# Kernel optimization log

Measured on AMD Instinct MI355X. Metric: run time of the kernel, lower is better.

The kernel has to match this reference:

```python
import jax, jax.numpy as jnp
import numpy as np

N_NODES = 100000
N_EDGES = 1600000
EMBED_DIM = 128
HIDDEN_DIM = 256


def setup_inputs() -> dict:
    key = jax.random.key(0)
    k_emb, k_src, k_dst, k_w1, k_w2 = jax.random.split(key, 5)
    emb = jax.random.normal(k_emb, (N_NODES, EMBED_DIM), dtype=jnp.float32)
    edge_src = jax.random.randint(k_src, (N_EDGES,), 0, N_NODES)
    edge_dst = jax.random.randint(k_dst, (N_EDGES,), 0, N_NODES)
    # Linear(2D -> H) and Linear(H -> D), stored as [in, out] for x @ W
    W1 = jax.random.normal(k_w1, (2 * EMBED_DIM, HIDDEN_DIM), dtype=jnp.float32) * (1.0 / np.sqrt(2 * EMBED_DIM))
    b1 = jnp.zeros((HIDDEN_DIM,), dtype=jnp.float32)
    W2 = jax.random.normal(k_w2, (HIDDEN_DIM, EMBED_DIM), dtype=jnp.float32) * (1.0 / np.sqrt(HIDDEN_DIM))
    b2 = jnp.zeros((EMBED_DIM,), dtype=jnp.float32)
    return {"emb": emb, "edge_src": edge_src, "edge_dst": edge_dst,
            "W1": W1, "b1": b1, "W2": W2, "b2": b2}


def reference(emb, edge_src, edge_dst, W1, b1, W2, b2):
    N, D = emb.shape
    E = edge_src.shape[0]
    # gather neighbor embeddings and segment-mean per destination node
    gathered = emb[edge_src]                                    # [E, D]
    nbr_sum = jax.ops.segment_sum(gathered, edge_dst, num_segments=N)   # [N, D]
    counts = jax.ops.segment_sum(jnp.ones((E,), emb.dtype), edge_dst, num_segments=N)  # [N]
    nbr_mean = nbr_sum / jnp.maximum(counts, 1.0)[:, None]
    # nodes with no neighbors fall back to their own embedding
    nbr_mean = jnp.where(counts[:, None] == 0, emb, nbr_mean)
    concat = jnp.concatenate([emb, nbr_mean], axis=-1)          # [N, 2D]
    h = jax.nn.relu(concat @ W1 + b1)                           # [N, H]
    return h @ W2 + b2                                          # [N, D]
```

## Files before the change

kernel.cpp:

```cpp
#include <hip/hip_runtime.h>

#define DD 128
#define HH 256
#define K1 256
#define BM 64
#define CH 2048
#define CH1 4096
#define CAP 8192

typedef __bf16 bf16;
typedef __attribute__((ext_vector_type(8))) __bf16 bf16x8;
typedef __attribute__((ext_vector_type(4))) float f32x4;
typedef __attribute__((ext_vector_type(2))) float f32x2;


__global__ __launch_bounds__(256) void count512_k(const int* __restrict__ dst,
                                                  int* __restrict__ bcnt,
                                                  int E, int BSH) {
    __shared__ int c[512];
    for (int j = threadIdx.x; j < 512; j += 256) c[j] = 0;
    __syncthreads();
    for (int e = blockIdx.x * 256 + threadIdx.x; e < E; e += gridDim.x * 256)
        atomicAdd(&c[dst[e] >> BSH], 1);
    __syncthreads();
    for (int j = threadIdx.x; j < 512; j += 256)
        if (c[j]) atomicAdd(&bcnt[j], c[j]);
}

__global__ __launch_bounds__(512) void scan512_k(const int* __restrict__ bcnt,
                                                 int* __restrict__ bbase,
                                                 int* __restrict__ bpos,
                                                 int NB, int E) {
    __shared__ int s[512];
    const int t = threadIdx.x;
    int v = (t < NB) ? bcnt[t] : 0;
    s[t] = v;
    __syncthreads();
    for (int off = 1; off < 512; off <<= 1) {
        int y = (t >= off) ? s[t - off] : 0;
        __syncthreads();
        s[t] += y;
        __syncthreads();
    }
    int excl = s[t] - v;
    if (t < NB) { bbase[t] = excl; bpos[t] = excl; }
    if (t == 0) bbase[NB] = E;
}

__global__ __launch_bounds__(256) void part512_k(const int* __restrict__ src,
                                                 const int* __restrict__ dst,
                                                 int* __restrict__ bpos,
                                                 int2* __restrict__ pairs,
                                                 int E, int BSH) {
    __shared__ int lcnt[512];
    __shared__ int lbase[512];
    const int t = threadIdx.x;
    const int e0 = blockIdx.x * CH1;
    const int e1 = min(E, e0 + CH1);
    for (int j = t; j < 512; j += 256) lcnt[j] = 0;
    __syncthreads();
    int rs[CH1 / 256];
    #pragma unroll
    for (int k = 0; k < CH1 / 256; ++k) {
        int e = e0 + k * 256 + t;
        int b = -1;
        if (e < e1) { b = dst[e] >> BSH; atomicAdd(&lcnt[b], 1); }
        rs[k] = b;
    }
    __syncthreads();
    for (int j = t; j < 512; j += 256) {
        int c = lcnt[j];
        lbase[j] = c ? atomicAdd(&bpos[j], c) : 0;
        lcnt[j] = 0;
    }
    __syncthreads();
    #pragma unroll
    for (int k = 0; k < CH1 / 256; ++k) {
        int e = e0 + k * 256 + t;
        if (e < e1) {
            int b = rs[k];
            int slot = lbase[b] + atomicAdd(&lcnt[b], 1);
            pairs[slot] = make_int2(src[e], dst[e]);
        }
    }
}

__global__ __launch_bounds__(256) void sortb_k(const int2* __restrict__ pairs,
                                               const int* __restrict__ bbase,
                                               int* __restrict__ offs,
                                               int* __restrict__ ssrc,
                                               int N, int BSH) {
    __shared__ int hist[512];
    __shared__ int pref[512];
    __shared__ int run[512];
    __shared__ int sorted[CAP];
    const int t = threadIdx.x;
    const int b = blockIdx.x;
    const int B = 1 << BSH;
    const int d0 = b << BSH;
    const int nd = min(B, N - d0);
    const int rb = bbase[b], re = bbase[b + 1];
    const int cntE = re - rb;
    for (int j = t; j < 512; j += 256) hist[j] = 0;
    __syncthreads();
    for (int i = rb + t; i < re; i += 256)
        atomicAdd(&hist[pairs[i].y - d0], 1);
    __syncthreads();
    for (int j = t; j < 512; j += 256) pref[j] = hist[j];
    __syncthreads();
    for (int off = 1; off < 512; off <<= 1) {
        int j2 = t + 256;
        int v0 = (t >= off) ? pref[t - off] : 0;
        int v1 = (j2 >= off) ? pref[j2 - off] : 0;
        __syncthreads();
        pref[t] += v0;
        pref[j2] += v1;
        __syncthreads();
    }
    for (int j = t; j < nd; j += 256) offs[d0 + j] = rb + pref[j];
    for (int j = t; j < 512; j += 256) run[j] = pref[j] - hist[j];
    __syncthreads();
    if (cntE <= CAP) {
        for (int i = rb + t; i < re; i += 256) {
            int2 p = pairs[i];
            int pos = atomicAdd(&run[p.y - d0], 1);
            sorted[pos] = p.x;
        }
        __syncthreads();
        for (int i = t; i < cntE; i += 256) ssrc[rb + i] = sorted[i];
    } else {
        for (int i = rb + t; i < re; i += 256) {
            int2 p = pairs[i];
            int pos = atomicAdd(&run[p.y - d0], 1);
            ssrc[rb + pos] = p.x;
        }
    }
}


__global__ __launch_bounds__(256) void hist_k(const int* __restrict__ dst,
                                              int* __restrict__ cnt, int E) {
    for (int e = blockIdx.x * blockDim.x + threadIdx.x; e < E;
         e += gridDim.x * blockDim.x)
        atomicAdd(&cnt[dst[e]], 1);
}

__global__ __launch_bounds__(256) void scan1_k(const int* __restrict__ cnt,
                                               int* __restrict__ offs,
                                               int* __restrict__ part, int N) {
    __shared__ int sdata[256];
    const int b = blockIdx.x, t = threadIdx.x;
    const int base = b * 1024 + t * 4;
    int v[4], sum = 0;
    #pragma unroll
    for (int i = 0; i < 4; ++i) {
        int idx = base + i;
        v[i] = (idx < N) ? cnt[idx] : 0;
        sum += v[i];
    }
    sdata[t] = sum;
    __syncthreads();
    for (int off = 1; off < 256; off <<= 1) {
        int y = (t >= off) ? sdata[t - off] : 0;
        __syncthreads();
        sdata[t] += y;
        __syncthreads();
    }
    int excl = sdata[t] - sum;
    if (t == 255) part[b] = sdata[255];
    int run = excl;
    #pragma unroll
    for (int i = 0; i < 4; ++i) {
        int idx = base + i;
        if (idx < N) offs[idx] = run;
        run += v[i];
    }
}

__global__ __launch_bounds__(128) void scan2_k(int* __restrict__ part, int nparts) {
    __shared__ int sdata[128];
    const int t = threadIdx.x;
    int v = (t < nparts) ? part[t] : 0;
    sdata[t] = v;
    __syncthreads();
    for (int off = 1; off < 128; off <<= 1) {
        int y = (t >= off) ? sdata[t - off] : 0;
        __syncthreads();
        sdata[t] += y;
        __syncthreads();
    }
    if (t < nparts) part[t] = sdata[t] - v;
}

__global__ __launch_bounds__(256) void scan3_k(int* __restrict__ offs,
                                               const int* __restrict__ part, int N) {
    for (int i = blockIdx.x * blockDim.x + threadIdx.x; i < N;
         i += gridDim.x * blockDim.x)
        offs[i] += part[i >> 10];
}

__global__ __launch_bounds__(256) void bucket_k(const int* __restrict__ src,
                                                const int* __restrict__ dst,
                                                int* __restrict__ offs,
                                                int* __restrict__ ssrc,
                                                int E, int N) {
    const int r = blockIdx.x & 7;
    const int chunk = blockIdx.x >> 3;
    const int lo = r * (N >> 3);
    const int hi = (r == 7) ? N : lo + (N >> 3);
    const int e0 = chunk * CH;
    const int e1 = min(E, e0 + CH);
    for (int e = e0 + threadIdx.x; e < e1; e += 256) {
        int d = dst[e];
        if (d >= lo && d < hi) {
            int pos = atomicAdd(&offs[d], 1);
            ssrc[pos] = src[e];
        }
    }
}

__global__ __launch_bounds__(256) void cvt8_k(const float* __restrict__ emb,
                                              unsigned* __restrict__ emb8,
                                              size_t n8) {
    for (size_t i = blockIdx.x * blockDim.x + threadIdx.x; i < n8;
         i += (size_t)gridDim.x * blockDim.x) {
        float4 a = *reinterpret_cast<const float4*>(&emb[i * 8]);
        float4 b = *reinterpret_cast<const float4*>(&emb[i * 8 + 4]);
        int w0 = __builtin_amdgcn_cvt_pk_fp8_f32(a.x, a.y, 0, false);
        w0 = __builtin_amdgcn_cvt_pk_fp8_f32(a.z, a.w, w0, true);
        int w1 = __builtin_amdgcn_cvt_pk_fp8_f32(b.x, b.y, 0, false);
        w1 = __builtin_amdgcn_cvt_pk_fp8_f32(b.z, b.w, w1, true);
        uint2 o; o.x = (unsigned)w0; o.y = (unsigned)w1;
        *reinterpret_cast<uint2*>(&emb8[i * 2]) = o;
    }
}

__global__ __launch_bounds__(256) void gather8_k(const unsigned* __restrict__ emb8,
                                                 const float* __restrict__ emb,
                                                 const int* __restrict__ offs,
                                                 const int* __restrict__ ssrc,
                                                 bf16* __restrict__ nbrh, int N) {
    const int wid = threadIdx.x >> 6;
    const int lane = threadIdx.x & 63;
    const int d = blockIdx.x * 4 + wid;
    if (d >= N) return;
    const int slot = lane >> 4;
    const int c8 = (lane & 15) * 8;
    const int start = (d == 0) ? 0 : offs[d - 1];
    const int end = offs[d];
    float acc[8];
    #pragma unroll
    for (int j = 0; j < 8; ++j) acc[j] = 0.f;
    int e = start;
    for (; e + 8 <= end; e += 8) {
        int s0 = ssrc[e + slot];
        int s1 = ssrc[e + 4 + slot];
        uint2 v0 = *reinterpret_cast<const uint2*>(&emb8[((size_t)s0 * DD + c8) >> 2]);
        uint2 v1 = *reinterpret_cast<const uint2*>(&emb8[((size_t)s1 * DD + c8) >> 2]);
        f32x2 p;
        p = __builtin_amdgcn_cvt_pk_f32_fp8(v0.x, false); acc[0] += p[0]; acc[1] += p[1];
        p = __builtin_amdgcn_cvt_pk_f32_fp8(v0.x, true);  acc[2] += p[0]; acc[3] += p[1];
        p = __builtin_amdgcn_cvt_pk_f32_fp8(v0.y, false); acc[4] += p[0]; acc[5] += p[1];
        p = __builtin_amdgcn_cvt_pk_f32_fp8(v0.y, true);  acc[6] += p[0]; acc[7] += p[1];
        p = __builtin_amdgcn_cvt_pk_f32_fp8(v1.x, false); acc[0] += p[0]; acc[1] += p[1];
        p = __builtin_amdgcn_cvt_pk_f32_fp8(v1.x, true);  acc[2] += p[0]; acc[3] += p[1];
        p = __builtin_amdgcn_cvt_pk_f32_fp8(v1.y, false); acc[4] += p[0]; acc[5] += p[1];
        p = __builtin_amdgcn_cvt_pk_f32_fp8(v1.y, true);  acc[6] += p[0]; acc[7] += p[1];
    }
    for (; e + 4 <= end; e += 4) {
        int s0 = ssrc[e + slot];
        uint2 v0 = *reinterpret_cast<const uint2*>(&emb8[((size_t)s0 * DD + c8) >> 2]);
        f32x2 p;
        p = __builtin_amdgcn_cvt_pk_f32_fp8(v0.x, false); acc[0] += p[0]; acc[1] += p[1];
        p = __builtin_amdgcn_cvt_pk_f32_fp8(v0.x, true);  acc[2] += p[0]; acc[3] += p[1];
        p = __builtin_amdgcn_cvt_pk_f32_fp8(v0.y, false); acc[4] += p[0]; acc[5] += p[1];
        p = __builtin_amdgcn_cvt_pk_f32_fp8(v0.y, true);  acc[6] += p[0]; acc[7] += p[1];
    }
    if (slot < end - e) {
        int s0 = ssrc[e + slot];
        uint2 v0 = *reinterpret_cast<const uint2*>(&emb8[((size_t)s0 * DD + c8) >> 2]);
        f32x2 p;
        p = __builtin_amdgcn_cvt_pk_f32_fp8(v0.x, false); acc[0] += p[0]; acc[1] += p[1];
        p = __builtin_amdgcn_cvt_pk_f32_fp8(v0.x, true);  acc[2] += p[0]; acc[3] += p[1];
        p = __builtin_amdgcn_cvt_pk_f32_fp8(v0.y, false); acc[4] += p[0]; acc[5] += p[1];
        p = __builtin_amdgcn_cvt_pk_f32_fp8(v0.y, true);  acc[6] += p[0]; acc[7] += p[1];
    }
    #pragma unroll
    for (int j = 0; j < 8; ++j) {
        acc[j] += __shfl_xor(acc[j], 16);
        acc[j] += __shfl_xor(acc[j], 32);
    }
    if (slot == 0) {
        bf16x8 o;
        if (end > start) {
            float inv = 1.f / (float)(end - start);
            #pragma unroll
            for (int j = 0; j < 8; ++j) o[j] = (bf16)(acc[j] * inv);
        } else {
            float4 a = *reinterpret_cast<const float4*>(&emb[(size_t)d * DD + c8]);
            float4 b = *reinterpret_cast<const float4*>(&emb[(size_t)d * DD + c8 + 4]);
            o[0]=(bf16)a.x; o[1]=(bf16)a.y; o[2]=(bf16)a.z; o[3]=(bf16)a.w;
            o[4]=(bf16)b.x; o[5]=(bf16)b.y; o[6]=(bf16)b.z; o[7]=(bf16)b.w;
        }
        *reinterpret_cast<bf16x8*>(&nbrh[(size_t)d * DD + c8]) = o;
    }
}

__global__ __launch_bounds__(256) void gather_k(const float* __restrict__ emb,
                                                const int* __restrict__ offs,
                                                const int* __restrict__ ssrc,
                                                float* __restrict__ nbr, int N) {
    const int wid = threadIdx.x >> 6;
    const int lane = threadIdx.x & 63;
    const int d = blockIdx.x * 4 + wid;
    if (d >= N) return;
    const int sub = lane >> 5;
    const int c = (lane & 31) * 4;
    const int start = (d == 0) ? 0 : offs[d - 1];
    const int end = offs[d];
    float4 acc = make_float4(0.f, 0.f, 0.f, 0.f);
    int e = start;
    for (; e + 4 <= end; e += 4) {
        int s0 = ssrc[e + sub];
        int s1 = ssrc[e + 2 + sub];
        float4 v0 = *reinterpret_cast<const float4*>(&emb[(size_t)s0 * DD + c]);
        float4 v1 = *reinterpret_cast<const float4*>(&emb[(size_t)s1 * DD + c]);
        acc.x += v0.x + v1.x; acc.y += v0.y + v1.y;
        acc.z += v0.z + v1.z; acc.w += v0.w + v1.w;
    }
    for (; e + 2 <= end; e += 2) {
        int s = ssrc[e + sub];
        float4 v = *reinterpret_cast<const float4*>(&emb[(size_t)s * DD + c]);
        acc.x += v.x; acc.y += v.y; acc.z += v.z; acc.w += v.w;
    }
    if (e < end && sub == 0) {
        int s = ssrc[e];
        float4 v = *reinterpret_cast<const float4*>(&emb[(size_t)s * DD + c]);
        acc.x += v.x; acc.y += v.y; acc.z += v.z; acc.w += v.w;
    }
    acc.x += __shfl_xor(acc.x, 32);
    acc.y += __shfl_xor(acc.y, 32);
    acc.z += __shfl_xor(acc.z, 32);
    acc.w += __shfl_xor(acc.w, 32);
    if (sub == 0) {
        if (end > start) {
            float inv = 1.f / (float)(end - start);
            acc.x *= inv; acc.y *= inv; acc.z *= inv; acc.w *= inv;
        } else {
            acc = *reinterpret_cast<const float4*>(&emb[(size_t)d * DD + c]);
        }
        *reinterpret_cast<float4*>(&nbr[(size_t)d * DD + c]) = acc;
    }
}

__global__ __launch_bounds__(64) void pack_k(const float* __restrict__ W, int NC,
                                             bf16* __restrict__ hi) {
    const int ntiles = NC >> 4;
    const int kt = blockIdx.x / ntiles;
    const int nt = blockIdx.x % ntiles;
    const int l = threadIdx.x;
    const int k0 = kt * 32 + (l >> 4) * 8;
    const int n = nt * 16 + (l & 15);
    bf16x8 hv;
    #pragma unroll
    for (int r = 0; r < 8; ++r)
        hv[r] = (bf16)W[(size_t)(k0 + r) * NC + n];
    *reinterpret_cast<bf16x8*>(hi + ((size_t)blockIdx.x * 64 + l) * 8) = hv;
}

__global__ __launch_bounds__(256) void mlp_mfma_k(const float* __restrict__ emb,
        const float* nbrf, const bf16* __restrict__ nbrh,
        const bf16* __restrict__ w1h, const float* __restrict__ b1,
        const bf16* __restrict__ w2h, const float* __restrict__ b2,
        float* out, int N) {
    __shared__ char smem[BM * K1 * 2];
    const int t = threadIdx.x;
    const int n0 = blockIdx.x * BM;
    const int l = t & 63;
    const int w = t >> 6;

    #pragma unroll
    for (int i = 0; i < 8; ++i) {
        int chunk = i * 256 + t;
        int row = chunk >> 5;
        int c0 = (chunk & 31) * 8;
        int n = n0 + row;
        bf16x8 hv;
        if (n < N) {
            if (c0 >= DD && nbrh != nullptr) {
                hv = *reinterpret_cast<const bf16x8*>(&nbrh[(size_t)n * DD + (c0 - DD)]);
            } else {
                const float* sp = (c0 < DD) ? &emb[(size_t)n * DD + c0]
                                            : &nbrf[(size_t)n * DD + (c0 - DD)];
                float4 a = *reinterpret_cast<const float4*>(sp);
                float4 b = *reinterpret_cast<const float4*>(sp + 4);
                hv[0]=(bf16)a.x; hv[1]=(bf16)a.y; hv[2]=(bf16)a.z; hv[3]=(bf16)a.w;
                hv[4]=(bf16)b.x; hv[5]=(bf16)b.y; hv[6]=(bf16)b.z; hv[7]=(bf16)b.w;
            }
        } else {
            #pragma unroll
            for (int j = 0; j < 8; ++j) hv[j] = (bf16)0.f;
        }
        int off = row * 512 + ((c0 * 2) ^ ((row & 7) << 4));
        *reinterpret_cast<bf16x8*>(smem + off) = hv;
    }
    __syncthreads();

    const int arow = l & 15;
    const int abyte = (l >> 4) * 16;

    f32x4 acc[4][4];
    #pragma unroll
    for (int ntl = 0; ntl < 4; ++ntl) {
        float bv = b1[w * 64 + ntl * 16 + (l & 15)];
        #pragma unroll
        for (int mt = 0; mt < 4; ++mt)
            acc[mt][ntl] = (f32x4){bv, bv, bv, bv};
    }
    for (int kt = 0; kt < 8; ++kt) {
        bf16x8 ah[4];
        #pragma unroll
        for (int mt = 0; mt < 4; ++mt) {
            int row = mt * 16 + arow;
            int off = row * 512 + ((kt * 64 + abyte) ^ ((row & 7) << 4));
            ah[mt] = *reinterpret_cast<const bf16x8*>(smem + off);
        }
        #pragma unroll
        for (int ntl = 0; ntl < 4; ++ntl) {
            int nt = w * 4 + ntl;
            size_t boff = ((size_t)(kt * 16 + nt) * 64 + l) * 8;
            bf16x8 bh = *reinterpret_cast<const bf16x8*>(w1h + boff);
            #pragma unroll
            for (int mt = 0; mt < 4; ++mt)
                acc[mt][ntl] = __builtin_amdgcn_mfma_f32_16x16x32_bf16(ah[mt], bh, acc[mt][ntl], 0, 0, 0);
        }
    }
    __syncthreads();

    #pragma unroll
    for (int mt = 0; mt < 4; ++mt)
        #pragma unroll
        for (int ntl = 0; ntl < 4; ++ntl) {
            int col = w * 64 + ntl * 16 + (l & 15);
            #pragma unroll
            for (int r = 0; r < 4; ++r) {
                int row = mt * 16 + (l >> 4) * 4 + r;
                int off = row * 512 + ((col * 2) ^ ((row & 7) << 4));
                *reinterpret_cast<bf16*>(smem + off) = (bf16)fmaxf(acc[mt][ntl][r], 0.f);
            }
        }
    __syncthreads();

    f32x4 acc2[4][2];
    #pragma unroll
    for (int ntl = 0; ntl < 2; ++ntl) {
        float bv = b2[w * 32 + ntl * 16 + (l & 15)];
        #pragma unroll
        for (int mt = 0; mt < 4; ++mt)
            acc2[mt][ntl] = (f32x4){bv, bv, bv, bv};
    }
    for (int kt = 0; kt < 8; ++kt) {
        bf16x8 ah[4];
        #pragma unroll
        for (int mt = 0; mt < 4; ++mt) {
            int row = mt * 16 + arow;
            int off = row * 512 + ((kt * 64 + abyte) ^ ((row & 7) << 4));
            ah[mt] = *reinterpret_cast<const bf16x8*>(smem + off);
        }
        #pragma unroll
        for (int ntl = 0; ntl < 2; ++ntl) {
            int nt = w * 2 + ntl;
            size_t boff = ((size_t)(kt * 8 + nt) * 64 + l) * 8;
            bf16x8 bh = *reinterpret_cast<const bf16x8*>(w2h + boff);
            #pragma unroll
            for (int mt = 0; mt < 4; ++mt)
                acc2[mt][ntl] = __builtin_amdgcn_mfma_f32_16x16x32_bf16(ah[mt], bh, acc2[mt][ntl], 0, 0, 0);
        }
    }
    #pragma unroll
    for (int mt = 0; mt < 4; ++mt)
        #pragma unroll
        for (int ntl = 0; ntl < 2; ++ntl) {
            int col = w * 32 + ntl * 16 + (l & 15);
            #pragma unroll
            for (int r = 0; r < 4; ++r) {
                int row = mt * 16 + (l >> 4) * 4 + r;
                int n = n0 + row;
                if (n < N) out[(size_t)n * DD + col] = acc2[mt][ntl][r];
            }
        }
}

__global__ __launch_bounds__(256) void scatter_k(const float* __restrict__ emb,
        const int* __restrict__ src, const int* __restrict__ dst,
        float* nbr, float* __restrict__ cnt, int E) {
    int e = blockIdx.x * 8 + (threadIdx.x >> 5);
    if (e >= E) return;
    int lane = threadIdx.x & 31;
    int s = src[e];
    int d = dst[e];
    const float4 v = *reinterpret_cast<const float4*>(&emb[(size_t)s * DD + lane * 4]);
    float* o = &nbr[(size_t)d * DD + lane * 4];
    atomicAdd(o + 0, v.x);
    atomicAdd(o + 1, v.y);
    atomicAdd(o + 2, v.z);
    atomicAdd(o + 3, v.w);
    if (lane == 0) atomicAdd(&cnt[d], 1.0f);
}

__global__ __launch_bounds__(256) void mlp_k(const float* __restrict__ emb,
        const float* nbr, const float* cnt,
        const float* __restrict__ W1, const float* __restrict__ b1,
        const float* __restrict__ W2, const float* __restrict__ b2,
        float* out, int N) {
    __shared__ float smem[BM * K1];
    const int t = threadIdx.x;
    const int n0 = blockIdx.x * BM;
    #pragma unroll
    for (int it = 0; it < 16; ++it) {
        int idx = it * 256 + t;
        int r = idx >> 6;
        int c4 = idx & 63;
        int n = n0 + r;
        float4 v = make_float4(0.f, 0.f, 0.f, 0.f);
        if (n < N) {
            if (c4 < 32) {
                v = *reinterpret_cast<const float4*>(&emb[(size_t)n * DD + c4 * 4]);
            } else {
                float c = cnt[n];
                if (c > 0.f) {
                    v = *reinterpret_cast<const float4*>(&nbr[(size_t)n * DD + (c4 - 32) * 4]);
                    float inv = 1.f / c;
                    v.x *= inv; v.y *= inv; v.z *= inv; v.w *= inv;
                } else {
                    v = *reinterpret_cast<const float4*>(&emb[(size_t)n * DD + (c4 - 32) * 4]);
                }
            }
        }
        *reinterpret_cast<float4*>(&smem[idx * 4]) = v;
    }
    __syncthreads();
    const int tx = t & 31;
    const int ty = t >> 5;
    const int r0 = ty * 8;
    {
        const int c0 = tx * 8;
        float acc[8][8];
        const float4 bva = *reinterpret_cast<const float4*>(&b1[c0]);
        const float4 bvb = *reinterpret_cast<const float4*>(&b1[c0 + 4]);
        #pragma unroll
        for (int i = 0; i < 8; ++i) {
            acc[i][0] = bva.x; acc[i][1] = bva.y; acc[i][2] = bva.z; acc[i][3] = bva.w;
            acc[i][4] = bvb.x; acc[i][5] = bvb.y; acc[i][6] = bvb.z; acc[i][7] = bvb.w;
        }
        for (int k0 = 0; k0 < K1; k0 += 4) {
            float xs[8][4];
            #pragma unroll
            for (int i = 0; i < 8; ++i) {
                float4 xv = *reinterpret_cast<const float4*>(&smem[(r0 + i) * K1 + k0]);
                xs[i][0] = xv.x; xs[i][1] = xv.y; xs[i][2] = xv.z; xs[i][3] = xv.w;
            }
            #pragma unroll
            for (int kk = 0; kk < 4; ++kk) {
                const float4 wa = *reinterpret_cast<const float4*>(&W1[(size_t)(k0 + kk) * HH + c0]);
                const float4 wb = *reinterpret_cast<const float4*>(&W1[(size_t)(k0 + kk) * HH + c0 + 4]);
                #pragma unroll
                for (int i = 0; i < 8; ++i) {
                    float x = xs[i][kk];
                    acc[i][0] += x * wa.x; acc[i][1] += x * wa.y;
                    acc[i][2] += x * wa.z; acc[i][3] += x * wa.w;
                    acc[i][4] += x * wb.x; acc[i][5] += x * wb.y;
                    acc[i][6] += x * wb.z; acc[i][7] += x * wb.w;
                }
            }
        }
        __syncthreads();
        #pragma unroll
        for (int i = 0; i < 8; ++i) {
            float4 h0, h1;
            h0.x = fmaxf(acc[i][0], 0.f); h0.y = fmaxf(acc[i][1], 0.f);
            h0.z = fmaxf(acc[i][2], 0.f); h0.w = fmaxf(acc[i][3], 0.f);
            h1.x = fmaxf(acc[i][4], 0.f); h1.y = fmaxf(acc[i][5], 0.f);
            h1.z = fmaxf(acc[i][6], 0.f); h1.w = fmaxf(acc[i][7], 0.f);
            *reinterpret_cast<float4*>(&smem[(r0 + i) * HH + c0]) = h0;
            *reinterpret_cast<float4*>(&smem[(r0 + i) * HH + c0 + 4]) = h1;
        }
        __syncthreads();
    }
    {
        const int c0 = tx * 4;
        float acc[8][4];
        const float4 bv = *reinterpret_cast<const float4*>(&b2[c0]);
        #pragma unroll
        for (int i = 0; i < 8; ++i) {
            acc[i][0] = bv.x; acc[i][1] = bv.y; acc[i][2] = bv.z; acc[i][3] = bv.w;
        }
        for (int k0 = 0; k0 < HH; k0 += 4) {
            float hs[8][4];
            #pragma unroll
            for (int i = 0; i < 8; ++i) {
                float4 hv = *reinterpret_cast<const float4*>(&smem[(r0 + i) * HH + k0]);
                hs[i][0] = hv.x; hs[i][1] = hv.y; hs[i][2] = hv.z; hs[i][3] = hv.w;
            }
            #pragma unroll
            for (int kk = 0; kk < 4; ++kk) {
                const float4 w2 = *reinterpret_cast<const float4*>(&W2[(size_t)(k0 + kk) * DD + c0]);
                #pragma unroll
                for (int i = 0; i < 8; ++i) {
                    float h = hs[i][kk];
                    acc[i][0] += h * w2.x; acc[i][1] += h * w2.y;
                    acc[i][2] += h * w2.z; acc[i][3] += h * w2.w;
                }
            }
        }
        #pragma unroll
        for (int i = 0; i < 8; ++i) {
            int n = n0 + r0 + i;
            if (n < N) {
                float4 o;
                o.x = acc[i][0]; o.y = acc[i][1]; o.z = acc[i][2]; o.w = acc[i][3];
                *reinterpret_cast<float4*>(&out[(size_t)n * DD + c0]) = o;
            }
        }
    }
}

extern "C" void kernel_launch(void* const* d_in, const int* in_sizes, int n_in,
                              void* d_out, int out_size, void* d_ws, size_t ws_size,
                              hipStream_t stream) {
    const float* emb = (const float*)d_in[0];
    const int* esrc  = (const int*)d_in[1];
    const int* edst  = (const int*)d_in[2];
    const float* W1  = (const float*)d_in[3];
    const float* b1  = (const float*)d_in[4];
    const float* W2  = (const float*)d_in[5];
    const float* b2  = (const float*)d_in[6];
    float* out = (float*)d_out;

    const int N = in_sizes[0] / DD;
    const int E = in_sizes[1];
    const int nparts = (N + 1023) / 1024;

    int BSH = 0;
    while ((((size_t)N + ((size_t)1 << BSH) - 1) >> BSH) > 512) ++BSH;
    const int B = 1 << BSH;
    const int NB = (N + B - 1) >> BSH;

    int* cnt  = (int*)d_ws;
    int* offs = cnt + N;
    int* part = offs + N;
    int* aux  = part + 128;
    int* ssrc = aux + 2048;
    char* wp = (char*)(ssrc + E);
    wp = (char*)(((uintptr_t)wp + 15) & ~(uintptr_t)15);
    bf16* w1h = (bf16*)wp;
    bf16* w2h = w1h + 65536;
    unsigned* emb8 = (unsigned*)(w2h + 32768);
    bf16* nbrh = (bf16*)(emb8 + (size_t)N * DD / 4);
    int2* pairs = (int2*)nbrh;
    int* bcnt  = aux;
    int* bbase = aux + 512;
    int* bpos  = aux + 1280;
    const size_t need_base = (size_t)((char*)(w2h + 32768) - (char*)d_ws);
    const size_t need_full = (size_t)((char*)(nbrh + (size_t)N * DD) - (char*)d_ws);
    const bool pairs_fit = ((size_t)E * sizeof(int2) <= (size_t)N * DD * sizeof(bf16));

    if (ws_size >= need_base && nparts <= 128) {
        const bool fast = (ws_size >= need_full) && pairs_fit && (B <= 512) && ((N & 7) == 0);
        pack_k<<<dim3(128), dim3(64), 0, stream>>>(W1, HH, w1h);
        pack_k<<<dim3(64), dim3(64), 0, stream>>>(W2, DD, w2h);
        if (fast) {
            hipMemsetAsync(bcnt, 0, 512 * sizeof(int), stream);
            count512_k<<<dim3(512), dim3(256), 0, stream>>>(edst, bcnt, E, BSH);
            scan512_k<<<dim3(1), dim3(512), 0, stream>>>(bcnt, bbase, bpos, NB, E);
            part512_k<<<dim3((E + CH1 - 1) / CH1), dim3(256), 0, stream>>>(
                esrc, edst, bpos, pairs, E, BSH);
            sortb_k<<<dim3(NB), dim3(256), 0, stream>>>(pairs, bbase, offs, ssrc, N, BSH);
            cvt8_k<<<dim3(2048), dim3(256), 0, stream>>>(emb, emb8, (size_t)N * DD / 8);
            gather8_k<<<dim3((N + 3) / 4), dim3(256), 0, stream>>>(emb8, emb, offs, ssrc, nbrh, N);
            mlp_mfma_k<<<dim3((N + BM - 1) / BM), dim3(256), 0, stream>>>(
                emb, nullptr, nbrh, w1h, b1, w2h, b2, out, N);
        } else {
            hipMemsetAsync(cnt, 0, (size_t)N * sizeof(int), stream);
            hist_k<<<dim3(1024), dim3(256), 0, stream>>>(edst, cnt, E);
            scan1_k<<<dim3(nparts), dim3(256), 0, stream>>>(cnt, offs, part, N);
            scan2_k<<<dim3(1), dim3(128), 0, stream>>>(part, nparts);
            scan3_k<<<dim3(512), dim3(256), 0, stream>>>(offs, part, N);
            const int nchunks = (E + CH - 1) / CH;
            bucket_k<<<dim3(nchunks * 8), dim3(256), 0, stream>>>(esrc, edst, offs, ssrc, E, N);
            gather_k<<<dim3((N + 3) / 4), dim3(256), 0, stream>>>(emb, offs, ssrc, out, N);
            mlp_mfma_k<<<dim3((N + BM - 1) / BM), dim3(256), 0, stream>>>(
                emb, out, nullptr, w1h, b1, w2h, b2, out, N);
        }
    } else {
        float* fcnt = (float*)d_ws;
        hipMemsetAsync(out, 0, (size_t)N * DD * sizeof(float), stream);
        hipMemsetAsync(fcnt, 0, (size_t)N * sizeof(float), stream);
        scatter_k<<<dim3((E + 7) / 8), dim3(256), 0, stream>>>(emb, esrc, edst, out, fcnt, E);
        mlp_k<<<dim3((N + BM - 1) / BM), dim3(256), 0, stream>>>(
            emb, out, fcnt, W1, b1, W2, b2, out, N);
    }
}
```

Before: 173.0 us.

## Fuse neighbor gather into MLP kernel and pack edge pairs into 32 bits

The fp8 neighbor gather/mean now runs inside the MLP kernel and writes straight into the shared-memory A tile, so the bf16 neighbor buffer round trip and one launch are gone. Edge pairs are packed into one 32-bit word (local dst in the top 8 bits, src in the low 24), which halves partition and sort traffic and lets pairs reuse the emb8 buffer. The two weight-pack launches are merged into one. In exchange, the gather now runs at one block per 64 nodes with serial iterations before the MFMA work, which may hide memory latency less well. The fast path is also limited to N < 2^24 and buckets of at most 256 nodes.

```diff
diff --git a/kernel.cpp b/kernel.cpp
--- a/kernel.cpp
+++ b/kernel.cpp
@@ -50,8 +50,8 @@
 __global__ __launch_bounds__(256) void part512_k(const int* __restrict__ src,
                                                  const int* __restrict__ dst,
                                                  int* __restrict__ bpos,
-                                                 int2* __restrict__ pairs,
-                                                 int E, int BSH) {
+                                                 unsigned* __restrict__ pairs,
+                                                 int E, int BSH, int Bm1) {
     __shared__ int lcnt[512];
     __shared__ int lbase[512];
     const int t = threadIdx.x;
@@ -80,12 +80,12 @@
         if (e < e1) {
             int b = rs[k];
             int slot = lbase[b] + atomicAdd(&lcnt[b], 1);
-            pairs[slot] = make_int2(src[e], dst[e]);
-        }
-    }
-}
-
-__global__ __launch_bounds__(256) void sortb_k(const int2* __restrict__ pairs,
+            pairs[slot] = ((unsigned)(dst[e] & Bm1) << 24) | (unsigned)src[e];
+        }
+    }
+}
+
+__global__ __launch_bounds__(256) void sortb_k(const unsigned* __restrict__ pairs,
                                                const int* __restrict__ bbase,
                                                int* __restrict__ offs,
                                                int* __restrict__ ssrc,
@@ -104,7 +104,7 @@
     for (int j = t; j < 512; j += 256) hist[j] = 0;
     __syncthreads();
     for (int i = rb + t; i < re; i += 256)
-        atomicAdd(&hist[pairs[i].y - d0], 1);
+        atomicAdd(&hist[pairs[i] >> 24], 1);
     __syncthreads();
     for (int j = t; j < 512; j += 256) pref[j] = hist[j];
     __syncthreads();
@@ -122,17 +122,17 @@
     __syncthreads();
     if (cntE <= CAP) {
         for (int i = rb + t; i < re; i += 256) {
-            int2 p = pairs[i];
-            int pos = atomicAdd(&run[p.y - d0], 1);
-            sorted[pos] = p.x;
+            unsigned p = pairs[i];
+            int pos = atomicAdd(&run[p >> 24], 1);
+            sorted[pos] = (int)(p & 0xFFFFFFu);
         }
         __syncthreads();
         for (int i = t; i < cntE; i += 256) ssrc[rb + i] = sorted[i];
     } else {
         for (int i = rb + t; i < re; i += 256) {
-            int2 p = pairs[i];
-            int pos = atomicAdd(&run[p.y - d0], 1);
-            ssrc[rb + pos] = p.x;
+            unsigned p = pairs[i];
+            int pos = atomicAdd(&run[p >> 24], 1);
+            ssrc[rb + pos] = (int)(p & 0xFFFFFFu);
         }
     }
 }
@@ -216,93 +216,6 @@
             int pos = atomicAdd(&offs[d], 1);
             ssrc[pos] = src[e];
         }
-    }
-}
-
-__global__ __launch_bounds__(256) void cvt8_k(const float* __restrict__ emb,
-                                              unsigned* __restrict__ emb8,
-                                              size_t n8) {
-    for (size_t i = blockIdx.x * blockDim.x + threadIdx.x; i < n8;
-         i += (size_t)gridDim.x * blockDim.x) {
-        float4 a = *reinterpret_cast<const float4*>(&emb[i * 8]);
-        float4 b = *reinterpret_cast<const float4*>(&emb[i * 8 + 4]);
-        int w0 = __builtin_amdgcn_cvt_pk_fp8_f32(a.x, a.y, 0, false);
-        w0 = __builtin_amdgcn_cvt_pk_fp8_f32(a.z, a.w, w0, true);
-        int w1 = __builtin_amdgcn_cvt_pk_fp8_f32(b.x, b.y, 0, false);
-        w1 = __builtin_amdgcn_cvt_pk_fp8_f32(b.z, b.w, w1, true);
-        uint2 o; o.x = (unsigned)w0; o.y = (unsigned)w1;
-        *reinterpret_cast<uint2*>(&emb8[i * 2]) = o;
-    }
-}
-
-__global__ __launch_bounds__(256) void gather8_k(const unsigned* __restrict__ emb8,
-                                                 const float* __restrict__ emb,
-                                                 const int* __restrict__ offs,
-                                                 const int* __restrict__ ssrc,
-                                                 bf16* __restrict__ nbrh, int N) {
-    const int wid = threadIdx.x >> 6;
-    const int lane = threadIdx.x & 63;
-    const int d = blockIdx.x * 4 + wid;
-    if (d >= N) return;
-    const int slot = lane >> 4;
-    const int c8 = (lane & 15) * 8;
-    const int start = (d == 0) ? 0 : offs[d - 1];
-    const int end = offs[d];
-    float acc[8];
-    #pragma unroll
-    for (int j = 0; j < 8; ++j) acc[j] = 0.f;
-    int e = start;
-    for (; e + 8 <= end; e += 8) {
-        int s0 = ssrc[e + slot];
-        int s1 = ssrc[e + 4 + slot];
-        uint2 v0 = *reinterpret_cast<const uint2*>(&emb8[((size_t)s0 * DD + c8) >> 2]);
-        uint2 v1 = *reinterpret_cast<const uint2*>(&emb8[((size_t)s1 * DD + c8) >> 2]);
-        f32x2 p;
-        p = __builtin_amdgcn_cvt_pk_f32_fp8(v0.x, false); acc[0] += p[0]; acc[1] += p[1];
-        p = __builtin_amdgcn_cvt_pk_f32_fp8(v0.x, true);  acc[2] += p[0]; acc[3] += p[1];
-        p = __builtin_amdgcn_cvt_pk_f32_fp8(v0.y, false); acc[4] += p[0]; acc[5] += p[1];
-        p = __builtin_amdgcn_cvt_pk_f32_fp8(v0.y, true);  acc[6] += p[0]; acc[7] += p[1];
-        p = __builtin_amdgcn_cvt_pk_f32_fp8(v1.x, false); acc[0] += p[0]; acc[1] += p[1];
-        p = __builtin_amdgcn_cvt_pk_f32_fp8(v1.x, true);  acc[2] += p[0]; acc[3] += p[1];
-        p = __builtin_amdgcn_cvt_pk_f32_fp8(v1.y, false); acc[4] += p[0]; acc[5] += p[1];
-        p = __builtin_amdgcn_cvt_pk_f32_fp8(v1.y, true);  acc[6] += p[0]; acc[7] += p[1];
-    }
-    for (; e + 4 <= end; e += 4) {
-        int s0 = ssrc[e + slot];
-        uint2 v0 = *reinterpret_cast<const uint2*>(&emb8[((size_t)s0 * DD + c8) >> 2]);
-        f32x2 p;
-        p = __builtin_amdgcn_cvt_pk_f32_fp8(v0.x, false); acc[0] += p[0]; acc[1] += p[1];
-        p = __builtin_amdgcn_cvt_pk_f32_fp8(v0.x, true);  acc[2] += p[0]; acc[3] += p[1];
-        p = __builtin_amdgcn_cvt_pk_f32_fp8(v0.y, false); acc[4] += p[0]; acc[5] += p[1];
-        p = __builtin_amdgcn_cvt_pk_f32_fp8(v0.y, true);  acc[6] += p[0]; acc[7] += p[1];
-    }
-    if (slot < end - e) {
-        int s0 = ssrc[e + slot];
-        uint2 v0 = *reinterpret_cast<const uint2*>(&emb8[((size_t)s0 * DD + c8) >> 2]);
-        f32x2 p;
-        p = __builtin_amdgcn_cvt_pk_f32_fp8(v0.x, false); acc[0] += p[0]; acc[1] += p[1];
-        p = __builtin_amdgcn_cvt_pk_f32_fp8(v0.x, true);  acc[2] += p[0]; acc[3] += p[1];
-        p = __builtin_amdgcn_cvt_pk_f32_fp8(v0.y, false); acc[4] += p[0]; acc[5] += p[1];
-        p = __builtin_amdgcn_cvt_pk_f32_fp8(v0.y, true);  acc[6] += p[0]; acc[7] += p[1];
-    }
-    #pragma unroll
-    for (int j = 0; j < 8; ++j) {
-        acc[j] += __shfl_xor(acc[j], 16);
-        acc[j] += __shfl_xor(acc[j], 32);
-    }
-    if (slot == 0) {
-        bf16x8 o;
-        if (end > start) {
-            float inv = 1.f / (float)(end - start);
-            #pragma unroll
-            for (int j = 0; j < 8; ++j) o[j] = (bf16)(acc[j] * inv);
-        } else {
-            float4 a = *reinterpret_cast<const float4*>(&emb[(size_t)d * DD + c8]);
-            float4 b = *reinterpret_cast<const float4*>(&emb[(size_t)d * DD + c8 + 4]);
-            o[0]=(bf16)a.x; o[1]=(bf16)a.y; o[2]=(bf16)a.z; o[3]=(bf16)a.w;
-            o[4]=(bf16)b.x; o[5]=(bf16)b.y; o[6]=(bf16)b.z; o[7]=(bf16)b.w;
-        }
-        *reinterpret_cast<bf16x8*>(&nbrh[(size_t)d * DD + c8]) = o;
     }
 }
 
@@ -353,11 +266,33 @@
     }
 }
 
-__global__ __launch_bounds__(64) void pack_k(const float* __restrict__ W, int NC,
-                                             bf16* __restrict__ hi) {
+__global__ __launch_bounds__(256) void cvt8_k(const float* __restrict__ emb,
+                                              unsigned* __restrict__ emb8,
+                                              size_t n8) {
+    for (size_t i = blockIdx.x * blockDim.x + threadIdx.x; i < n8;
+         i += (size_t)gridDim.x * blockDim.x) {
+        float4 a = *reinterpret_cast<const float4*>(&emb[i * 8]);
+        float4 b = *reinterpret_cast<const float4*>(&emb[i * 8 + 4]);
+        int w0 = __builtin_amdgcn_cvt_pk_fp8_f32(a.x, a.y, 0, false);
+        w0 = __builtin_amdgcn_cvt_pk_fp8_f32(a.z, a.w, w0, true);
+        int w1 = __builtin_amdgcn_cvt_pk_fp8_f32(b.x, b.y, 0, false);
+        w1 = __builtin_amdgcn_cvt_pk_fp8_f32(b.z, b.w, w1, true);
+        uint2 o; o.x = (unsigned)w0; o.y = (unsigned)w1;
+        *reinterpret_cast<uint2*>(&emb8[i * 2]) = o;
+    }
+}
+
+__global__ __launch_bounds__(64) void packW_k(const float* __restrict__ W1,
+                                              const float* __restrict__ W2,
+                                              bf16* __restrict__ w1h,
+                                              bf16* __restrict__ w2h) {
+    const int bid = blockIdx.x;
+    const float* W; bf16* outp; int NC; int rel;
+    if (bid < 128) { W = W1; outp = w1h; NC = HH; rel = bid; }
+    else           { W = W2; outp = w2h; NC = DD; rel = bid - 128; }
     const int ntiles = NC >> 4;
-    const int kt = blockIdx.x / ntiles;
-    const int nt = blockIdx.x % ntiles;
+    const int kt = rel / ntiles;
+    const int nt = rel % ntiles;
     const int l = threadIdx.x;
     const int k0 = kt * 32 + (l >> 4) * 8;
     const int n = nt * 16 + (l & 15);
@@ -365,11 +300,201 @@
     #pragma unroll
     for (int r = 0; r < 8; ++r)
         hv[r] = (bf16)W[(size_t)(k0 + r) * NC + n];
-    *reinterpret_cast<bf16x8*>(hi + ((size_t)blockIdx.x * 64 + l) * 8) = hv;
+    *reinterpret_cast<bf16x8*>(outp + ((size_t)rel * 64 + l) * 8) = hv;
+}
+
+__global__ __launch_bounds__(256) void mlp_fused_k(const float* __restrict__ emb,
+        const unsigned* __restrict__ emb8,
+        const int* __restrict__ offs, const int* __restrict__ ssrc,
+        const bf16* __restrict__ w1h, const float* __restrict__ b1,
+        const bf16* __restrict__ w2h, const float* __restrict__ b2,
+        float* __restrict__ out, int N) {
+    __shared__ char smem[BM * K1 * 2];
+    const int t = threadIdx.x;
+    const int n0 = blockIdx.x * BM;
+    const int l = t & 63;
+    const int w = t >> 6;
+
+    #pragma unroll
+    for (int i = 0; i < 4; ++i) {
+        int chunk = i * 256 + t;
+        int row = chunk >> 4;
+        int c0 = (chunk & 15) * 8;
+        int n = n0 + row;
+        bf16x8 hv;
+        if (n < N) {
+            float4 a = *reinterpret_cast<const float4*>(&emb[(size_t)n * DD + c0]);
+            float4 b = *reinterpret_cast<const float4*>(&emb[(size_t)n * DD + c0 + 4]);
+            hv[0]=(bf16)a.x; hv[1]=(bf16)a.y; hv[2]=(bf16)a.z; hv[3]=(bf16)a.w;
+            hv[4]=(bf16)b.x; hv[5]=(bf16)b.y; hv[6]=(bf16)b.z; hv[7]=(bf16)b.w;
+        } else {
+            #pragma unroll
+            for (int j = 0; j < 8; ++j) hv[j] = (bf16)0.f;
+        }
+        int off = row * 512 + ((c0 * 2) ^ ((row & 7) << 4));
+        *reinterpret_cast<bf16x8*>(smem + off) = hv;
+    }
+
+    {
+        const int slot = l >> 4;
+        const int c8 = (l & 15) * 8;
+        for (int it = 0; it < 16; ++it) {
+            int row = it * 4 + w;
+            int d = n0 + row;
+            bf16x8 o;
+            #pragma unroll
+            for (int j = 0; j < 8; ++j) o[j] = (bf16)0.f;
+            if (d < N) {
+                const int start = (d == 0) ? 0 : offs[d - 1];
+                const int end = offs[d];
+                float acc[8];
+                #pragma unroll
+                for (int j = 0; j < 8; ++j) acc[j] = 0.f;
+                int e = start;
+                for (; e + 8 <= end; e += 8) {
+                    int s0 = ssrc[e + slot];
+                    int s1 = ssrc[e + 4 + slot];
+                    uint2 v0 = *reinterpret_cast<const uint2*>(&emb8[((size_t)s0 * DD + c8) >> 2]);
+                    uint2 v1 = *reinterpret_cast<const uint2*>(&emb8[((size_t)s1 * DD + c8) >> 2]);
+                    f32x2 p;
+                    p = __builtin_amdgcn_cvt_pk_f32_fp8(v0.x, false); acc[0] += p[0]; acc[1] += p[1];
+                    p = __builtin_amdgcn_cvt_pk_f32_fp8(v0.x, true);  acc[2] += p[0]; acc[3] += p[1];
+                    p = __builtin_amdgcn_cvt_pk_f32_fp8(v0.y, false); acc[4] += p[0]; acc[5] += p[1];
+                    p = __builtin_amdgcn_cvt_pk_f32_fp8(v0.y, true);  acc[6] += p[0]; acc[7] += p[1];
+                    p = __builtin_amdgcn_cvt_pk_f32_fp8(v1.x, false); acc[0] += p[0]; acc[1] += p[1];
+                    p = __builtin_amdgcn_cvt_pk_f32_fp8(v1.x, true);  acc[2] += p[0]; acc[3] += p[1];
+                    p = __builtin_amdgcn_cvt_pk_f32_fp8(v1.y, false); acc[4] += p[0]; acc[5] += p[1];
+                    p = __builtin_amdgcn_cvt_pk_f32_fp8(v1.y, true);  acc[6] += p[0]; acc[7] += p[1];
+                }
+                for (; e + 4 <= end; e += 4) {
+                    int s0 = ssrc[e + slot];
+                    uint2 v0 = *reinterpret_cast<const uint2*>(&emb8[((size_t)s0 * DD + c8) >> 2]);
+                    f32x2 p;
+                    p = __builtin_amdgcn_cvt_pk_f32_fp8(v0.x, false); acc[0] += p[0]; acc[1] += p[1];
+                    p = __builtin_amdgcn_cvt_pk_f32_fp8(v0.x, true);  acc[2] += p[0]; acc[3] += p[1];
+                    p = __builtin_amdgcn_cvt_pk_f32_fp8(v0.y, false); acc[4] += p[0]; acc[5] += p[1];
+                    p = __builtin_amdgcn_cvt_pk_f32_fp8(v0.y, true);  acc[6] += p[0]; acc[7] += p[1];
+                }
+                if (slot < end - e) {
+                    int s0 = ssrc[e + slot];
+                    uint2 v0 = *reinterpret_cast<const uint2*>(&emb8[((size_t)s0 * DD + c8) >> 2]);
+                    f32x2 p;
+                    p = __builtin_amdgcn_cvt_pk_f32_fp8(v0.x, false); acc[0] += p[0]; acc[1] += p[1];
+                    p = __builtin_amdgcn_cvt_pk_f32_fp8(v0.x, true);  acc[2] += p[0]; acc[3] += p[1];
+                    p = __builtin_amdgcn_cvt_pk_f32_fp8(v0.y, false); acc[4] += p[0]; acc[5] += p[1];
+                    p = __builtin_amdgcn_cvt_pk_f32_fp8(v0.y, true);  acc[6] += p[0]; acc[7] += p[1];
+                }
+                #pragma unroll
+                for (int j = 0; j < 8; ++j) {
+                    acc[j] += __shfl_xor(acc[j], 16);
+                    acc[j] += __shfl_xor(acc[j], 32);
+                }
+                if (end > start) {
+                    float inv = 1.f / (float)(end - start);
+                    #pragma unroll
+                    for (int j = 0; j < 8; ++j) o[j] = (bf16)(acc[j] * inv);
+                } else {
+                    float4 a = *reinterpret_cast<const float4*>(&emb[(size_t)d * DD + c8]);
+                    float4 b = *reinterpret_cast<const float4*>(&emb[(size_t)d * DD + c8 + 4]);
+                    o[0]=(bf16)a.x; o[1]=(bf16)a.y; o[2]=(bf16)a.z; o[3]=(bf16)a.w;
+                    o[4]=(bf16)b.x; o[5]=(bf16)b.y; o[6]=(bf16)b.z; o[7]=(bf16)b.w;
+                }
+            }
+            if (slot == 0) {
+                int off = row * 512 + (((DD + c8) * 2) ^ ((row & 7) << 4));
+                *reinterpret_cast<bf16x8*>(smem + off) = o;
+            }
+        }
+    }
+    __syncthreads();
+
+    const int arow = l & 15;
+    const int abyte = (l >> 4) * 16;
+
+    f32x4 acc[4][4];
+    #pragma unroll
+    for (int ntl = 0; ntl < 4; ++ntl) {
+        float bv = b1[w * 64 + ntl * 16 + (l & 15)];
+        #pragma unroll
+        for (int mt = 0; mt < 4; ++mt)
+            acc[mt][ntl] = (f32x4){bv, bv, bv, bv};
+    }
+    for (int kt = 0; kt < 8; ++kt) {
+        bf16x8 ah[4];
+        #pragma unroll
+        for (int mt = 0; mt < 4; ++mt) {
+            int row = mt * 16 + arow;
+            int off = row * 512 + ((kt * 64 + abyte) ^ ((row & 7) << 4));
+            ah[mt] = *reinterpret_cast<const bf16x8*>(smem + off);
+        }
+        #pragma unroll
+        for (int ntl = 0; ntl < 4; ++ntl) {
+            int nt = w * 4 + ntl;
+            size_t boff = ((size_t)(kt * 16 + nt) * 64 + l) * 8;
+            bf16x8 bh = *reinterpret_cast<const bf16x8*>(w1h + boff);
+            #pragma unroll
+            for (int mt = 0; mt < 4; ++mt)
+                acc[mt][ntl] = __builtin_amdgcn_mfma_f32_16x16x32_bf16(ah[mt], bh, acc[mt][ntl], 0, 0, 0);
+        }
+    }
+    __syncthreads();
+
+    #pragma unroll
+    for (int mt = 0; mt < 4; ++mt)
+        #pragma unroll
+        for (int ntl = 0; ntl < 4; ++ntl) {
+            int col = w * 64 + ntl * 16 + (l & 15);
+            #pragma unroll
+            for (int r = 0; r < 4; ++r) {
+                int row = mt * 16 + (l >> 4) * 4 + r;
+                int off = row * 512 + ((col * 2) ^ ((row & 7) << 4));
+                *reinterpret_cast<bf16*>(smem + off) = (bf16)fmaxf(acc[mt][ntl][r], 0.f);
+            }
+        }
+    __syncthreads();
+
+    f32x4 acc2[4][2];
+    #pragma unroll
+    for (int ntl = 0; ntl < 2; ++ntl) {
+        float bv = b2[w * 32 + ntl * 16 + (l & 15)];
+        #pragma unroll
+        for (int mt = 0; mt < 4; ++mt)
+            acc2[mt][ntl] = (f32x4){bv, bv, bv, bv};
+    }
+    for (int kt = 0; kt < 8; ++kt) {
+        bf16x8 ah[4];
+        #pragma unroll
+        for (int mt = 0; mt < 4; ++mt) {
+            int row = mt * 16 + arow;
+            int off = row * 512 + ((kt * 64 + abyte) ^ ((row & 7) << 4));
+            ah[mt] = *reinterpret_cast<const bf16x8*>(smem + off);
+        }
+        #pragma unroll
+        for (int ntl = 0; ntl < 2; ++ntl) {
+            int nt = w * 2 + ntl;
+            size_t boff = ((size_t)(kt * 8 + nt) * 64 + l) * 8;
+            bf16x8 bh = *reinterpret_cast<const bf16x8*>(w2h + boff);
+            #pragma unroll
+            for (int mt = 0; mt < 4; ++mt)
+                acc2[mt][ntl] = __builtin_amdgcn_mfma_f32_16x16x32_bf16(ah[mt], bh, acc2[mt][ntl], 0, 0, 0);
+        }
+    }
+    #pragma unroll
+    for (int mt = 0; mt < 4; ++mt)
+        #pragma unroll
+        for (int ntl = 0; ntl < 2; ++ntl) {
+            int col = w * 32 + ntl * 16 + (l & 15);
+            #pragma unroll
+            for (int r = 0; r < 4; ++r) {
+                int row = mt * 16 + (l >> 4) * 4 + r;
+                int n = n0 + row;
+                if (n < N) out[(size_t)n * DD + col] = acc2[mt][ntl][r];
+            }
+        }
 }
 
 __global__ __launch_bounds__(256) void mlp_mfma_k(const float* __restrict__ emb,
-        const float* nbrf, const bf16* __restrict__ nbrh,
+        const float* nbrf,
         const bf16* __restrict__ w1h, const float* __restrict__ b1,
         const bf16* __restrict__ w2h, const float* __restrict__ b2,
         float* out, int N) {
@@ -387,16 +512,12 @@
         int n = n0 + row;
         bf16x8 hv;
         if (n < N) {
-            if (c0 >= DD && nbrh != nullptr) {
-                hv = *reinterpret_cast<const bf16x8*>(&nbrh[(size_t)n * DD + (c0 - DD)]);
-            } else {
-                const float* sp = (c0 < DD) ? &emb[(size_t)n * DD + c0]
-                                            : &nbrf[(size_t)n * DD + (c0 - DD)];
-                float4 a = *reinterpret_cast<const float4*>(sp);
-                float4 b = *reinterpret_cast<const float4*>(sp + 4);
-                hv[0]=(bf16)a.x; hv[1]=(bf16)a.y; hv[2]=(bf16)a.z; hv[3]=(bf16)a.w;
-                hv[4]=(bf16)b.x; hv[5]=(bf16)b.y; hv[6]=(bf16)b.z; hv[7]=(bf16)b.w;
-            }
+            const float* sp = (c0 < DD) ? &emb[(size_t)n * DD + c0]
+                                        : &nbrf[(size_t)n * DD + (c0 - DD)];
+            float4 a = *reinterpret_cast<const float4*>(sp);
+            float4 b = *reinterpret_cast<const float4*>(sp + 4);
+            hv[0]=(bf16)a.x; hv[1]=(bf16)a.y; hv[2]=(bf16)a.z; hv[3]=(bf16)a.w;
+            hv[4]=(bf16)b.x; hv[5]=(bf16)b.y; hv[6]=(bf16)b.z; hv[7]=(bf16)b.w;
         } else {
             #pragma unroll
             for (int j = 0; j < 8; ++j) hv[j] = (bf16)0.f;
@@ -436,7 +557,6 @@
         }
     }
     __syncthreads();
-
     #pragma unroll
     for (int mt = 0; mt < 4; ++mt)
         #pragma unroll
@@ -656,30 +776,28 @@
     bf16* w1h = (bf16*)wp;
     bf16* w2h = w1h + 65536;
     unsigned* emb8 = (unsigned*)(w2h + 32768);
-    bf16* nbrh = (bf16*)(emb8 + (size_t)N * DD / 4);
-    int2* pairs = (int2*)nbrh;
+    unsigned* pairs = emb8;
     int* bcnt  = aux;
     int* bbase = aux + 512;
     int* bpos  = aux + 1280;
     const size_t need_base = (size_t)((char*)(w2h + 32768) - (char*)d_ws);
-    const size_t need_full = (size_t)((char*)(nbrh + (size_t)N * DD) - (char*)d_ws);
-    const bool pairs_fit = ((size_t)E * sizeof(int2) <= (size_t)N * DD * sizeof(bf16));
+    const size_t need_full = (size_t)((char*)(emb8 + (size_t)N * DD / 4) - (char*)d_ws);
+    const bool pairs_fit = ((size_t)E <= (size_t)N * DD / 4);
 
     if (ws_size >= need_base && nparts <= 128) {
-        const bool fast = (ws_size >= need_full) && pairs_fit && (B <= 512) && ((N & 7) == 0);
-        pack_k<<<dim3(128), dim3(64), 0, stream>>>(W1, HH, w1h);
-        pack_k<<<dim3(64), dim3(64), 0, stream>>>(W2, DD, w2h);
+        const bool fast = (ws_size >= need_full) && pairs_fit && (BSH <= 8) &&
+                          (N < (1 << 24)) && ((N & 7) == 0);
+        packW_k<<<dim3(192), dim3(64), 0, stream>>>(W1, W2, w1h, w2h);
         if (fast) {
             hipMemsetAsync(bcnt, 0, 512 * sizeof(int), stream);
             count512_k<<<dim3(512), dim3(256), 0, stream>>>(edst, bcnt, E, BSH);
             scan512_k<<<dim3(1), dim3(512), 0, stream>>>(bcnt, bbase, bpos, NB, E);
             part512_k<<<dim3((E + CH1 - 1) / CH1), dim3(256), 0, stream>>>(
-                esrc, edst, bpos, pairs, E, BSH);
+                esrc, edst, bpos, pairs, E, BSH, B - 1);
             sortb_k<<<dim3(NB), dim3(256), 0, stream>>>(pairs, bbase, offs, ssrc, N, BSH);
             cvt8_k<<<dim3(2048), dim3(256), 0, stream>>>(emb, emb8, (size_t)N * DD / 8);
-            gather8_k<<<dim3((N + 3) / 4), dim3(256), 0, stream>>>(emb8, emb, offs, ssrc, nbrh, N);
-            mlp_mfma_k<<<dim3((N + BM - 1) / BM), dim3(256), 0, stream>>>(
-                emb, nullptr, nbrh, w1h, b1, w2h, b2, out, N);
+            mlp_fused_k<<<dim3((N + BM - 1) / BM), dim3(256), 0, stream>>>(
+                emb, emb8, offs, ssrc, w1h, b1, w2h, b2, out, N);
         } else {
             hipMemsetAsync(cnt, 0, (size_t)N * sizeof(int), stream);
             hist_k<<<dim3(1024), dim3(256), 0, stream>>>(edst, cnt, E);
@@ -690,7 +808,7 @@
             bucket_k<<<dim3(nchunks * 8), dim3(256), 0, stream>>>(esrc, edst, offs, ssrc, E, N);
             gather_k<<<dim3((N + 3) / 4), dim3(256), 0, stream>>>(emb, offs, ssrc, out, N);
             mlp_mfma_k<<<dim3((N + BM - 1) / BM), dim3(256), 0, stream>>>(
-                emb, out, nullptr, w1h, b1, w2h, b2, out, N);
+                emb, out, w1h, b1, w2h, b2, out, N);
         }
     } else {
         float* fcnt = (float*)d_ws;
```

New measurement: 235.4 us. +36.1%, slower.
